# Kernel optimization log

Measured on AMD Instinct MI355X. Metric: run time of the kernel, lower is better.

Reference implementation:

```python
import jax, jax.numpy as jnp
import numpy as np

B, NBV, VD, A = 65536, 56, 7, 81
_BN_INV = np.float32(1.0 / np.sqrt(1.0 + 1e-5))  # eval-mode BN, running mean=0 var=1 (init state)


def _bn(x, g, b):
    # x: [B, C, F], per-channel affine over axis -2
    return x * (g * _BN_INV)[:, None] + b[:, None]


def _dpg(x, W, b, ng=8, ni=8):
    # DenseAndPartialGPool: first ng*ni feats -> grouped max+avg pool, rest -> relu(Linear)
    grp = x[..., : ng * ni].reshape(x.shape[:-1] + (ng, ni))
    dense = jax.nn.relu(x[..., ng * ni :] @ W + b)
    return jnp.concatenate([grp.max(-1), grp.mean(-1), dense], -1)


def setup_inputs() -> dict:
    key = jax.random.key(0)
    ks = iter(jax.random.split(key, 80))

    def W(si, so):
        return jax.random.normal(next(ks), (si, so), jnp.float32) * np.float32(1.0 / np.sqrt(si))

    def bias(n):
        return jnp.full((n,), 0.01, jnp.float32)

    inp = {}
    inp["input_data"] = jax.random.normal(next(ks), (B, NBV, VD), jnp.float32)
    inp["valid_actions"] = jax.random.randint(next(ks), (B, 1, A), 0, 2) > 0
    # dense2d_1
    inp["W1"], inp["b1"], inp["g1"], inp["be1"] = W(NBV, 128), bias(128), jnp.ones((7,), jnp.float32), jnp.zeros((7,), jnp.float32)
    inp["W2"], inp["b2"], inp["g2"], inp["be2"] = W(128, 128), bias(128), jnp.ones((7,), jnp.float32), jnp.zeros((7,), jnp.float32)
    inp["Wp1"], inp["bp1"] = W(64, 112), bias(112)
    inp["W3"], inp["b3"], inp["g3"], inp["be3"] = W(128, 128), bias(128), jnp.ones((7,), jnp.float32), jnp.zeros((7,), jnp.float32)
    inp["Wp2"], inp["bp2"] = W(64, 112), bias(112)
    inp["W4"], inp["b4"], inp["g4"], inp["be4"] = W(128, 128), bias(128), jnp.ones((7,), jnp.float32), jnp.zeros((7,), jnp.float32)
    inp["W5"], inp["b5"], inp["g5"], inp["be5"] = W(704, 512), bias(512), jnp.ones((1,), jnp.float32), jnp.zeros((1,), jnp.float32)
    inp["W6"], inp["b6"], inp["g6"], inp["be6"] = W(512, 256), bias(256), jnp.ones((1,), jnp.float32), jnp.zeros((1,), jnp.float32)
    inp["Wp4"], inp["bp4"] = W(192, 240), bias(240)
    inp["W7"], inp["b7"], inp["g7"], inp["be7"] = W(256, 256), bias(256), jnp.ones((1,), jnp.float32), jnp.zeros((1,), jnp.float32)
    inp["W8"], inp["b8"], inp["g8"], inp["be8"] = W(256, 256), bias(256), jnp.ones((1,), jnp.float32), jnp.zeros((1,), jnp.float32)
    inp["Wp5"], inp["bp5"] = W(192, 240), bias(240)
    inp["Wpi1"], inp["bpi1"] = W(256, 256), bias(256)
    inp["Wpi2"], inp["bpi2"] = W(256, A), bias(A)
    inp["Wv1"], inp["bv1"] = W(256, 256), bias(256)
    inp["Wv2"], inp["bv2"] = W(256, 1), bias(1)
    return inp


def reference(input_data, valid_actions, W1, b1, g1, be1, W2, b2, g2, be2, Wp1, bp1,
              W3, b3, g3, be3, Wp2, bp2, W4, b4, g4, be4,
              W5, b5, g5, be5, W6, b6, g6, be6, Wp4, bp4,
              W7, b7, g7, be7, W8, b8, g8, be8, Wp5, bp5,
              Wpi1, bpi1, Wpi2, bpi2, Wv1, bv1, Wv2, bv2):
    relu = jax.nn.relu
    x = jnp.transpose(input_data, (0, 2, 1))          # [B, 7, 56]
    x = relu(_bn(x @ W1 + b1, g1, be1))               # [B, 7, 128]
    x = relu(_bn(x @ W2 + b2, g2, be2))
    x = _dpg(x, Wp1, bp1)                             # [B, 7, 128]
    x = relu(_bn(x @ W3 + b3, g3, be3))
    x = _dpg(x, Wp2, bp2)
    x = relu(_bn(x @ W4 + b4, g4, be4))               # [B, 7, 128]
    # FlattenAndPartialGPool(64, 5)
    xb, xe = x[:, :, :64], x[:, :, 64:]
    first = xb[:, :5, :]                              # [B, 5, 64]
    n = x.shape[0]
    x = jnp.concatenate([first.max(1), first.mean(1),
                         xb[:, 5:, :].reshape(n, -1), xe.reshape(n, -1)], -1)[:, None, :]  # [B,1,704]
    x = relu(_bn(x @ W5 + b5, g5, be5))               # [B, 1, 512]
    x = relu(_bn(x @ W6 + b6, g6, be6))               # [B, 1, 256]
    x = _dpg(x, Wp4, bp4)
    x = relu(_bn(x @ W7 + b7, g7, be7))
    x = relu(_bn(x @ W8 + b8, g8, be8))
    x = _dpg(x, Wp5, bp5)                             # [B, 1, 256]
    v = jnp.tanh((x @ Wv1 + bv1) @ Wv2 + bv2)         # [B, 1, 1]
    pi = (x @ Wpi1 + bpi1) @ Wpi2 + bpi2              # [B, 1, A]
    pi = jnp.where(valid_actions, pi, jnp.float32(-1e8))
    return jax.nn.log_softmax(pi, axis=-1)[:, 0, :], v[:, 0, 0]
```

## Files before the change

### kernel.cpp

```cpp
#include <hip/hip_runtime.h>
#include <hip/hip_bf16.h>
#include <math.h>

#define BN_INV 0.99999500003749966f
#define NEG_BIG (-100000000.0f)

typedef __attribute__((ext_vector_type(8))) short s16x8;
typedef __attribute__((ext_vector_type(4))) float f32x4;

#define MFMA16(a,b,c) __builtin_amdgcn_mfma_f32_16x16x32_bf16(a,b,c,0,0,0)

__device__ __forceinline__ ushort f2b(float f){
  unsigned u = __builtin_bit_cast(unsigned, f);
  unsigned r = (u + 0x7FFFu + ((u>>16)&1u)) >> 16;
  return (ushort)r;
}
__device__ __forceinline__ float b2f(ushort h){
  unsigned u = ((unsigned)h)<<16; return __builtin_bit_cast(float, u);
}

#define OFF_W1   0
#define OFF_W2   8192
#define OFF_W3   24576
#define OFF_W4   40960
#define OFF_WP1  57344
#define OFF_WP2  64512
#define OFF_W5   71680
#define OFF_W6   432128
#define OFF_WP4  563200
#define OFF_WP5  609280
#define OFF_W7   655360
#define OFF_W8   720896
#define OFF_WPI1 786432
#define OFF_WPI2 851968
#define OFF_WV1  876544
#define OFF_X    942080

struct PrepParams {
  const float* src[15];
  long long off[15];
  int K[15], N[15], Kp[15], Np[15];
  ushort* ws;
};

__global__ void prep_pack(PrepParams pp){
  int wi = blockIdx.y;
  const float* s = pp.src[wi];
  ushort* d = pp.ws + pp.off[wi];
  int K = pp.K[wi], N = pp.N[wi], Np = pp.Np[wi];
  int tot = pp.Kp[wi]*Np;
  for (int idx = blockIdx.x*blockDim.x + threadIdx.x; idx < tot; idx += gridDim.x*blockDim.x){
    int k = idx / Np, j = idx - k*Np;
    float v = (k < K && j < N) ? s[k*N + j] : 0.f;
    d[(((k>>3)*Np + j)<<3) + (k&7)] = f2b(v);
  }
}

#define S1 136

struct P1 {
  const float* inp; const ushort* ws; ushort* xout;
  const float *b1,*g1,*be1,*b2,*g2,*be2,*bp1,*b3,*g3,*be3,*bp2,*b4,*g4,*be4;
};

template<int KT>
__device__ __forceinline__ void p1_mm(const ushort* X, ushort* Y, const ushort* W,
    const float* bias, const float* g, const float* be, int t){
  const int l=t&63, w=t>>6, lo=l&15, hi=l>>4;
  s16x8 Bf[2][KT];
  #pragma unroll
  for (int nt=0;nt<2;nt++)
    #pragma unroll
    for (int kt=0;kt<KT;kt++)
      Bf[nt][kt] = *(const s16x8*)(W + (((kt*4+hi)*128 + (w*2+nt)*16 + lo)<<3));
  float bc0 = bias[(w*2)*16+lo], bc1 = bias[(w*2+1)*16+lo];
  for (int mt=0; mt<7; mt++){
    const int rowb = mt*16;
    s16x8 Af[KT];
    #pragma unroll
    for (int kt=0;kt<KT;kt++)
      Af[kt] = *(const s16x8*)(X + (rowb+lo)*S1 + kt*32 + hi*8);
    f32x4 a0 = {0.f,0.f,0.f,0.f}, a1 = {0.f,0.f,0.f,0.f};
    #pragma unroll
    for (int kt=0;kt<KT;kt++){
      a0 = MFMA16(Af[kt], Bf[0][kt], a0);
      a1 = MFMA16(Af[kt], Bf[1][kt], a1);
    }
    #pragma unroll
    for (int r=0;r<4;r++){
      int row = rowb + hi*4 + r;
      int j = row % 7;
      float scj = g[j]*BN_INV, bbj = be[j];
      float v0 = fmaxf((a0[r]+bc0)*scj + bbj, 0.f);
      float v1 = fmaxf((a1[r]+bc1)*scj + bbj, 0.f);
      Y[row*S1 + (w*2)*16 + lo]   = f2b(v0);
      Y[row*S1 + (w*2+1)*16 + lo] = f2b(v1);
    }
  }
}

__device__ __forceinline__ void p1_dpg(const ushort* X, ushort* Y, const ushort* Wp,
                                       const float* bp, int t){
  const int l=t&63, w=t>>6, lo=l&15, hi=l>>4;
  const int nt0 = 2*w;
  const int ntn = (w<3) ? 2 : 1;
  s16x8 Bf[2][2];
  #pragma unroll
  for (int nt=0;nt<2;nt++)
    if (nt < ntn)
      #pragma unroll
      for (int kt=0;kt<2;kt++)
        Bf[nt][kt] = *(const s16x8*)(Wp + (((kt*4+hi)*112 + (nt0+nt)*16 + lo)<<3));
  float bc[2];
  #pragma unroll
  for (int nt=0;nt<2;nt++) bc[nt] = (nt<ntn) ? bp[(nt0+nt)*16+lo] : 0.f;
  for (int mt=0; mt<7; mt++){
    const int rowb = mt*16;
    s16x8 Af[2];
    #pragma unroll
    for (int kt=0;kt<2;kt++)
      Af[kt] = *(const s16x8*)(X + (rowb+lo)*S1 + 64 + kt*32 + hi*8);
    f32x4 acc0 = {0.f,0.f,0.f,0.f}, acc1 = {0.f,0.f,0.f,0.f};
    #pragma unroll
    for (int kt=0;kt<2;kt++){
      acc0 = MFMA16(Af[kt], Bf[0][kt], acc0);
      if (ntn > 1) acc1 = MFMA16(Af[kt], Bf[1][kt], acc1);
    }
    #pragma unroll
    for (int r=0;r<4;r++){
      int row = rowb + hi*4 + r;
      Y[row*S1 + 16 + nt0*16 + lo] = f2b(fmaxf(acc0[r] + bc[0], 0.f));
      if (ntn > 1)
        Y[row*S1 + 16 + (nt0+1)*16 + lo] = f2b(fmaxf(acc1[r] + bc[1], 0.f));
    }
  }
  if (w == 3){
    #pragma unroll
    for (int i=0;i<14;i++){
      int tau = l + 64*i;
      int row = tau>>3, gg = tau&7;
      s16x8 v8 = *(const s16x8*)(X + row*S1 + gg*8);
      float mx = b2f((ushort)v8[0]), smv = mx;
      #pragma unroll
      for (int q2=1;q2<8;q2++){ float vv = b2f((ushort)v8[q2]); mx = fmaxf(mx,vv); smv += vv; }
      Y[row*S1 + gg]     = f2b(mx);
      Y[row*S1 + 8 + gg] = f2b(smv*0.125f);
    }
  }
}

__global__ __launch_bounds__(256,2) void p1_kernel(P1 P){
  __shared__ ushort sA[112*S1];
  __shared__ ushort sB[112*S1];
  const int t = threadIdx.x;
  const size_t b0 = (size_t)blockIdx.x*16;
  const float* ip = P.inp + b0*392;
  for (int f=t; f<16*392; f+=256){
    int e = f/392, rem = f - e*392;
    int i = rem/7, j = rem - i*7;
    sA[(e*7+j)*S1 + i] = f2b(ip[f]);
  }
  for (int idx=t; idx<112*8; idx+=256)
    sA[(idx>>3)*S1 + 56 + (idx&7)] = 0;
  __syncthreads();
  p1_mm<2>(sA,sB, P.ws+OFF_W1, P.b1,P.g1,P.be1, t); __syncthreads();
  p1_mm<4>(sB,sA, P.ws+OFF_W2, P.b2,P.g2,P.be2, t); __syncthreads();
  p1_dpg(sA,sB, P.ws+OFF_WP1, P.bp1, t);            __syncthreads();
  p1_mm<4>(sB,sA, P.ws+OFF_W3, P.b3,P.g3,P.be3, t); __syncthreads();
  p1_dpg(sA,sB, P.ws+OFF_WP2, P.bp2, t);            __syncthreads();
  p1_mm<4>(sB,sA, P.ws+OFF_W4, P.b4,P.g4,P.be4, t); __syncthreads();
  ushort* xo = P.xout + b0*704;
  for (int idx=t; idx<16*704; idx+=256){
    int e = idx/704, c = idx - e*704;
    const ushort* Xr = sA + e*7*S1;
    float v;
    if (c < 64){
      float mx = b2f(Xr[c]);
      #pragma unroll
      for (int j=1;j<5;j++) mx = fmaxf(mx, b2f(Xr[j*S1+c]));
      v = mx;
    } else if (c < 128){
      int cc = c-64; float smv = 0.f;
      #pragma unroll
      for (int j=0;j<5;j++) smv += b2f(Xr[j*S1+cc]);
      v = smv*0.2f;
    } else if (c < 192) v = b2f(Xr[5*S1 + c-128]);
    else if (c < 256)   v = b2f(Xr[6*S1 + c-192]);
    else { int q2 = c-256; v = b2f(Xr[(q2>>6)*S1 + 64 + (q2&63)]); }
    xo[idx] = f2b(v);
  }
}

#define SX 712
#define SY 520
#define SZ 264

struct P2 {
  const ushort* x; const ushort* ws; const void* valid;
  const float *b5,*g5,*be5,*b6,*g6,*be6,*bp4,*b7,*g7,*be7,*b8,*g8,*be8,*bp5;
  const float *bpi1,*bpi2,*bv1,*Wv2,*bv2;
  float* out; long long Btot;
};

template<int KT, int NTW, int WN, int MODE>
__device__ __forceinline__ void p2_mm(const ushort* X, int sx, int xoff,
    ushort* Y, int sy, int yoff, const ushort* W, int n0,
    const float* bias, int bmax, float sc, float bb, int lo, int hi, int nact)
{
  f32x4 acc[4][NTW];
  #pragma unroll
  for (int m=0;m<4;m++)
    #pragma unroll
    for (int n=0;n<NTW;n++)
      acc[m][n] = (f32x4){0.f,0.f,0.f,0.f};
  for (int kt=0; kt<KT; kt++){
    s16x8 Af[4];
    #pragma unroll
    for (int m=0;m<4;m++)
      Af[m] = *(const s16x8*)(X + (m*16+lo)*sx + xoff + kt*32 + hi*8);
    s16x8 Bf[NTW];
    #pragma unroll
    for (int n=0;n<NTW;n++)
      if (n < nact)
        Bf[n] = *(const s16x8*)(W + (((size_t)(kt*4+hi)*WN + n0 + n*16 + lo)<<3));
    #pragma unroll
    for (int m=0;m<4;m++)
      #pragma unroll
      for (int n=0;n<NTW;n++)
        if (n < nact)
          acc[m][n] = MFMA16(Af[m], Bf[n], acc[m][n]);
  }
  #pragma unroll
  for (int n=0;n<NTW;n++){
    if (n < nact){
      int colw = n0 + n*16 + lo;
      float bc = (colw < bmax) ? bias[colw] : 0.f;
      #pragma unroll
      for (int m=0;m<4;m++){
        #pragma unroll
        for (int r=0;r<4;r++){
          int row = m*16 + hi*4 + r;
          float v = acc[m][n][r] + bc;
          if (MODE==0) v = fmaxf(v*sc+bb, 0.f);
          else if (MODE==1) v = fmaxf(v, 0.f);
          if (MODE==3) ((float*)Y)[row*sy + yoff + colw] = v;
          else Y[row*sy + yoff + colw] = f2b(v);
        }
      }
    }
  }
}

__device__ __forceinline__ void p2_group(const ushort* X, ushort* Y, int t){
  int row = t>>3, gg = t&7;
  s16x8 v8 = *(const s16x8*)(X + row*SZ + gg*8);
  float mx = b2f((ushort)v8[0]), smv = mx;
  #pragma unroll
  for (int q2=1;q2<8;q2++){ float vv = b2f((ushort)v8[q2]); mx = fmaxf(mx,vv); smv += vv; }
  Y[row*SZ + gg]     = f2b(mx);
  Y[row*SZ + 8 + gg] = f2b(smv*0.125f);
}

__global__ __launch_bounds__(512,2) void p2_kernel(P2 P){
  __shared__ ushort sm[78848];
  __shared__ int sflags[2];
  ushort* A0 = sm;
  ushort* A1 = sm + 45568;
  ushort* B0 = sm;
  ushort* B1 = sm + 16896;
  ushort* C  = sm + 45568;
  float*  Lf = (float*)sm;
  const int t = threadIdx.x;
  const int l = t&63, w = t>>6, lo = l&15, hi = l>>4;
  const size_t b0 = (size_t)blockIdx.x * 64;

  if (t < 2) sflags[t] = 0;
  __syncthreads();
  if (t < 256){
    const unsigned* vw = (const unsigned*)P.valid;
    int f3=0, nz=0;
    #pragma unroll
    for (int i=0;i<4;i++){
      unsigned u = vw[t*4+i];
      if (u & 0xFFFFFF00u) nz=1;
      if (((u>>24)&0xFFu)==0x3Fu || ((u>>16)&0xFFu)==0x3Fu ||
          ((u>>8)&0xFFu)==0x3Fu  || (u&0xFFu)==0x3Fu) f3=1;
    }
    if (f3) atomicOr(&sflags[0],1);
    if (nz) atomicOr(&sflags[1],1);
  }
  const ushort* xi = P.x + b0*704;
  for (int ci = t; ci < 64*88; ci += 512){
    int row = ci/88, c8 = ci - row*88;
    *(s16x8*)(A0 + row*SX + c8*8) = *(const s16x8*)(xi + row*704 + c8*8);
  }
  __syncthreads();
  const int vmode = sflags[0] ? 2 : (sflags[1] ? 0 : 1);
  float sc, bb;
  sc = P.g5[0]*BN_INV; bb = P.be5[0];
  p2_mm<22,4,512,0>(A0,SX,0, A1,SY,0, P.ws+OFF_W5, w*64, P.b5,512, sc,bb, lo,hi, 4);
  __syncthreads();
  sc = P.g6[0]*BN_INV; bb = P.be6[0];
  p2_mm<16,2,256,0>(A1,SY,0, B0,SZ,0, P.ws+OFF_W6, w*32, P.b6,256, sc,bb, lo,hi, 2);
  __syncthreads();
  p2_group(B0, B1, t);
  p2_mm<6,2,240,1>(B0,SZ,64, B1,SZ,16, P.ws+OFF_WP4, w*32, P.bp4,240, 0.f,0.f, lo,hi, (w==7)?1:2);
  __syncthreads();
  sc = P.g7[0]*BN_INV; bb = P.be7[0];
  p2_mm<8,2,256,0>(B1,SZ,0, B0,SZ,0, P.ws+OFF_W7, w*32, P.b7,256, sc,bb, lo,hi, 2);
  __syncthreads();
  sc = P.g8[0]*BN_INV; bb = P.be8[0];
  p2_mm<8,2,256,0>(B0,SZ,0, B1,SZ,0, P.ws+OFF_W8, w*32, P.b8,256, sc,bb, lo,hi, 2);
  __syncthreads();
  p2_group(B1, B0, t);
  p2_mm<6,2,240,1>(B1,SZ,64, B0,SZ,16, P.ws+OFF_WP5, w*32, P.bp5,240, 0.f,0.f, lo,hi, (w==7)?1:2);
  __syncthreads();
  p2_mm<8,2,256,2>(B0,SZ,0, B1,SZ,0, P.ws+OFF_WPI1, w*32, P.bpi1,256, 0.f,0.f, lo,hi, 2);
  p2_mm<8,2,256,2>(B0,SZ,0, C ,SZ,0, P.ws+OFF_WV1,  w*32, P.bv1, 256, 0.f,0.f, lo,hi, 2);
  __syncthreads();
  if (w < 6){
    p2_mm<8,1,96,3>(B1,SZ,0, (ushort*)Lf,104,0, P.ws+OFF_WPI2, w*16, P.bpi2,81, 0.f,0.f, lo,hi, 1);
  } else {
    int idx = (w-6)*64 + l;
    int row = idx>>1, half = idx&1;
    const ushort* hv = C + row*SZ + half*128;
    float s = 0.f;
    for (int k=0;k<128;k++) s += b2f(hv[k]) * P.Wv2[half*128+k];
    s += __shfl_xor(s, 1);
    if (!half) P.out[(size_t)P.Btot*81 + b0 + row] = tanhf(s + P.bv2[0]);
  }
  __syncthreads();
  {
    int row = t>>3, q = t&7;
    size_t b = b0 + row;
    const float* lr = Lf + row*104;
    float pm[11]; float mx = -INFINITY;
    #pragma unroll
    for (int i=0;i<11;i++){
      int c = q + 8*i;
      float v = NEG_BIG;
      if (c < 81){
        float sv = lr[c];
        bool valid;
        size_t vidx = b*81 + c;
        if (vmode==0)      valid = ((const unsigned char*)P.valid)[vidx] != 0;
        else if (vmode==1) valid = ((const int*)P.valid)[vidx] != 0;
        else               valid = ((const float*)P.valid)[vidx] != 0.f;
        v = valid ? sv : NEG_BIG;
      }
      pm[i] = v;
      mx = fmaxf(mx, v);
    }
    #pragma unroll
    for (int o=4;o;o>>=1) mx = fmaxf(mx, __shfl_xor(mx, o));
    float se = 0.f;
    #pragma unroll
    for (int i=0;i<11;i++){
      int c = q + 8*i;
      if (c < 81) se += expf(pm[i]-mx);
    }
    #pragma unroll
    for (int o=4;o;o>>=1) se += __shfl_xor(se, o);
    float lse = mx + logf(se);
    #pragma unroll
    for (int i=0;i<11;i++){
      int c = q + 8*i;
      if (c < 81) P.out[b*81 + c] = pm[i] - lse;
    }
  }
}

struct Params {
  const float* input;
  const void*  valid;
  const float *W1,*b1,*g1,*be1, *W2,*b2,*g2,*be2, *Wp1,*bp1;
  const float *W3,*b3,*g3,*be3, *Wp2,*bp2, *W4,*b4,*g4,*be4;
  const float *W5,*b5,*g5,*be5, *W6,*b6,*g6,*be6, *Wp4,*bp4;
  const float *W7,*b7,*g7,*be7, *W8,*b8,*g8,*be8, *Wp5,*bp5;
  const float *Wpi1,*bpi1,*Wpi2,*bpi2, *Wv1,*bv1,*Wv2,*bv2;
  float* out;
};

template<int K>
__device__ __forceinline__ void mm_p1(const float* __restrict__ X, float* __restrict__ Y,
    const float* __restrict__ W, const float* __restrict__ bias,
    const float* __restrict__ g, const float* __restrict__ be){
  const int t = threadIdx.x;
  const int m = t & 31, e = t >> 5;
  const int c0 = m * 4;
  const float* Xr = X + e*7*128;
  float acc[7][4];
  #pragma unroll
  for (int j=0;j<7;j++){acc[j][0]=0.f;acc[j][1]=0.f;acc[j][2]=0.f;acc[j][3]=0.f;}
  for (int k=0;k<K;k+=4){
    float4 wv[4];
    #pragma unroll
    for (int kk=0;kk<4;kk++) wv[kk] = *(const float4*)(W + (k+kk)*128 + c0);
    #pragma unroll
    for (int j=0;j<7;j++){
      float4 xv = *(const float4*)(Xr + j*128 + k);
      float xx[4] = {xv.x, xv.y, xv.z, xv.w};
      #pragma unroll
      for (int kk=0;kk<4;kk++){
        acc[j][0] += xx[kk]*wv[kk].x; acc[j][1] += xx[kk]*wv[kk].y;
        acc[j][2] += xx[kk]*wv[kk].z; acc[j][3] += xx[kk]*wv[kk].w;
      }
    }
  }
  float4 bs = *(const float4*)(bias + c0);
  #pragma unroll
  for (int j=0;j<7;j++){
    float sc = g[j]*BN_INV; float bb = be[j];
    float4 o;
    o.x = fmaxf((acc[j][0]+bs.x)*sc + bb, 0.f);
    o.y = fmaxf((acc[j][1]+bs.y)*sc + bb, 0.f);
    o.z = fmaxf((acc[j][2]+bs.z)*sc + bb, 0.f);
    o.w = fmaxf((acc[j][3]+bs.w)*sc + bb, 0.f);
    *(float4*)(Y + (e*7+j)*128 + c0) = o;
  }
}

__device__ __forceinline__ void dpg_p1f(const float* __restrict__ X, float* __restrict__ Y,
    const float* __restrict__ Wp, const float* __restrict__ bp){
  const int t = threadIdx.x;
  const int m = t & 31, e = t >> 5;
  const float* Xr = X + e*7*128;
  float* Yr = Y + e*7*128;
  if (m < 28) {
    const int c0 = m*4;
    float acc[7][4];
    #pragma unroll
    for (int j=0;j<7;j++){acc[j][0]=0.f;acc[j][1]=0.f;acc[j][2]=0.f;acc[j][3]=0.f;}
    for (int k=0;k<64;k+=4){
      float4 wv[4];
      #pragma unroll
      for (int kk=0;kk<4;kk++) wv[kk] = *(const float4*)(Wp + (k+kk)*112 + c0);
      #pragma unroll
      for (int j=0;j<7;j++){
        float4 xv = *(const float4*)(Xr + j*128 + 64 + k);
        float xx[4] = {xv.x, xv.y, xv.z, xv.w};
        #pragma unroll
        for (int kk=0;kk<4;kk++){
          acc[j][0] += xx[kk]*wv[kk].x; acc[j][1] += xx[kk]*wv[kk].y;
          acc[j][2] += xx[kk]*wv[kk].z; acc[j][3] += xx[kk]*wv[kk].w;
        }
      }
    }
    float4 bs = *(const float4*)(bp + c0);
    #pragma unroll
    for (int j=0;j<7;j++){
      float4 o;
      o.x = fmaxf(acc[j][0]+bs.x, 0.f); o.y = fmaxf(acc[j][1]+bs.y, 0.f);
      o.z = fmaxf(acc[j][2]+bs.z, 0.f); o.w = fmaxf(acc[j][3]+bs.w, 0.f);
      *(float4*)(Yr + j*128 + 16 + c0) = o;
    }
  } else if (m < 30) {
    #pragma unroll
    for (int j=0;j<7;j++){
      #pragma unroll
      for (int gi=0; gi<4; gi++){
        int gg = (m-28)*4 + gi;
        const float* p = Xr + j*128 + gg*8;
        float mx = p[0], smv = p[0];
        #pragma unroll
        for (int i=1;i<8;i++){ float v = p[i]; mx = fmaxf(mx, v); smv += v; }
        Yr[j*128 + gg] = mx;
        Yr[j*128 + 8 + gg] = smv*0.125f;
      }
    }
  }
}

__device__ __forceinline__ void flatten_st(const float* __restrict__ X, float* __restrict__ F){
  const int t = threadIdx.x, m = t & 31, e = t >> 5;
  const float* Xr = X + e*7*128;
  float* Fr = F + e*704;
  for (int col=m; col<704; col+=32){
    float v;
    if (col < 64){
      float mx = Xr[col];
      #pragma unroll
      for (int j=1;j<5;j++) mx = fmaxf(mx, Xr[j*128+col]);
      v = mx;
    } else if (col < 128){
      int c = col-64; float smv = 0.f;
      #pragma unroll
      for (int j=0;j<5;j++) smv += Xr[j*128+c];
      v = smv*0.2f;
    } else if (col < 192){ v = Xr[5*128 + (col-128)];
    } else if (col < 256){ v = Xr[6*128 + (col-192)];
    } else { int q = col-256; v = Xr[(q>>6)*128 + 64 + (q&63)]; }
    Fr[col] = v;
  }
}

template<int K, int N, int RPG, int MODE>
__device__ __forceinline__ void mm_p2(const float* __restrict__ X, int sx,
    float* __restrict__ Y, int sy, const float* __restrict__ W,
    const float* __restrict__ bias, float sc, float bb){
  constexpr int NC4 = N/4;
  constexpr int NG  = (8 + RPG - 1) / RPG;
  const int t = threadIdx.x;
  const int ci = t % NC4;
  const int grp = t / NC4;
  if (grp < NG) {
    const int c0 = ci*4;
    const int r0 = grp*RPG;
    float acc[RPG][4];
    #pragma unroll
    for (int r=0;r<RPG;r++){acc[r][0]=0.f;acc[r][1]=0.f;acc[r][2]=0.f;acc[r][3]=0.f;}
    for (int k=0;k<K;k+=4){
      float4 wv[4];
      #pragma unroll
      for (int kk=0;kk<4;kk++) wv[kk] = *(const float4*)(W + (k+kk)*N + c0);
      #pragma unroll
      for (int r=0;r<RPG;r++){
        float4 xv = *(const float4*)(X + (r0+r)*sx + k);
        float xx[4] = {xv.x, xv.y, xv.z, xv.w};
        #pragma unroll
        for (int kk=0;kk<4;kk++){
          acc[r][0] += xx[kk]*wv[kk].x; acc[r][1] += xx[kk]*wv[kk].y;
          acc[r][2] += xx[kk]*wv[kk].z; acc[r][3] += xx[kk]*wv[kk].w;
        }
      }
    }
    float4 bs = *(const float4*)(bias + c0);
    #pragma unroll
    for (int r=0;r<RPG;r++){
      float o[4] = {acc[r][0]+bs.x, acc[r][1]+bs.y, acc[r][2]+bs.z, acc[r][3]+bs.w};
      #pragma unroll
      for (int q=0;q<4;q++){
        if (MODE == 0) o[q] = o[q]*sc + bb;
        if (MODE <= 1) o[q] = fmaxf(o[q], 0.f);
      }
      float4 ov = {o[0],o[1],o[2],o[3]};
      *(float4*)(Y + (r0+r)*sy + c0) = ov;
    }
  }
}

__device__ __forceinline__ void dpg_p2_group(const float* __restrict__ X, float* __restrict__ Y){
  const int t = threadIdx.x;
  if (t < 128){
    int r = t >> 4, g0 = t & 15;
    const float* p = X + r*256 + (g0&7)*8;
    float mx = p[0], smv = p[0];
    #pragma unroll
    for (int i=1;i<8;i++){ float v = p[i]; mx = fmaxf(mx, v); smv += v; }
    Y[r*256 + g0] = (g0 < 8) ? mx : smv*0.125f;
  }
}

__global__ __launch_bounds__(256, 2)
void splendor_fwd(Params P, int Bt)
{
  __shared__ float bufA[7168];
  __shared__ float bufB[7168];
  __shared__ int sflags[2];
  const int t = threadIdx.x;
  const int b0 = blockIdx.x * 8;

  if (t < 2) sflags[t] = 0;
  __syncthreads();
  {
    const unsigned int* vw = (const unsigned int*)P.valid;
    int f3 = 0, nz = 0;
    #pragma unroll
    for (int i=0;i<4;i++){
      unsigned int u = vw[t*4 + i];
      if (u & 0xFFFFFF00u) nz = 1;
      if (((u>>24)&0xFFu)==0x3Fu || ((u>>16)&0xFFu)==0x3Fu ||
          ((u>>8)&0xFFu)==0x3Fu  || (u&0xFFu)==0x3Fu) f3 = 1;
    }
    if (f3) atomicOr(&sflags[0], 1);
    if (nz) atomicOr(&sflags[1], 1);
  }
  {
    const float* inp = P.input + (size_t)b0*392;
    for (int f=t; f<3136; f+=256){
      int e = f/392, rem = f - e*392;
      int i = rem/7, j = rem - i*7;
      bufA[(e*7+j)*128 + i] = inp[f];
    }
  }
  __syncthreads();
  const int vmode = sflags[0] ? 2 : (sflags[1] ? 0 : 1);

  mm_p1<56>(bufA, bufB, P.W1, P.b1, P.g1, P.be1);   __syncthreads();
  mm_p1<128>(bufB, bufA, P.W2, P.b2, P.g2, P.be2);  __syncthreads();
  dpg_p1f(bufA, bufB, P.Wp1, P.bp1);                __syncthreads();
  mm_p1<128>(bufB, bufA, P.W3, P.b3, P.g3, P.be3);  __syncthreads();
  dpg_p1f(bufA, bufB, P.Wp2, P.bp2);                __syncthreads();
  mm_p1<128>(bufB, bufA, P.W4, P.b4, P.g4, P.be4);  __syncthreads();
  flatten_st(bufA, bufB);                           __syncthreads();

  mm_p2<704,512,4,0>(bufB,704, bufA,512, P.W5, P.b5, P.g5[0]*BN_INV, P.be5[0]); __syncthreads();
  mm_p2<512,256,2,0>(bufA,512, bufB,256, P.W6, P.b6, P.g6[0]*BN_INV, P.be6[0]); __syncthreads();
  mm_p2<192,240,2,1>(bufB+64,256, bufA+16,256, P.Wp4, P.bp4, 0.f, 0.f);
  dpg_p2_group(bufB, bufA);                         __syncthreads();
  mm_p2<256,256,2,0>(bufA,256, bufB,256, P.W7, P.b7, P.g7[0]*BN_INV, P.be7[0]); __syncthreads();
  mm_p2<256,256,2,0>(bufB,256, bufA,256, P.W8, P.b8, P.g8[0]*BN_INV, P.be8[0]); __syncthreads();
  mm_p2<192,240,2,1>(bufA+64,256, bufB+16,256, P.Wp5, P.bp5, 0.f, 0.f);
  dpg_p2_group(bufA, bufB);                         __syncthreads();
  mm_p2<256,256,2,2>(bufB,256, bufA,256,      P.Wpi1, P.bpi1, 0.f, 0.f);
  mm_p2<256,256,2,2>(bufB,256, bufA+2048,256, P.Wv1,  P.bv1,  0.f, 0.f);
  __syncthreads();

  {
    const int r = t >> 5, lq = t & 31;
    const int b = b0 + r;
    const float* hp = bufA + r*256;
    float pm[3] = {NEG_BIG, NEG_BIG, NEG_BIG};
    float mx = -INFINITY;
    #pragma unroll
    for (int p=0;p<3;p++){
      int c = lq + 32*p;
      if (c < 81){
        float s = P.bpi2[c];
        for (int k=0;k<256;k++) s += hp[k]*P.Wpi2[k*81+c];
        bool valid;
        size_t idx = (size_t)b*81 + c;
        if (vmode == 0)      valid = ((const unsigned char*)P.valid)[idx] != 0;
        else if (vmode == 1) valid = ((const int*)P.valid)[idx] != 0;
        else                 valid = ((const float*)P.valid)[idx] != 0.f;
        pm[p] = valid ? s : NEG_BIG;
        mx = fmaxf(mx, pm[p]);
      }
    }
    #pragma unroll
    for (int off=16;off;off>>=1) mx = fmaxf(mx, __shfl_xor(mx, off, 32));
    float se = 0.f;
    #pragma unroll
    for (int p=0;p<3;p++){
      int c = lq + 32*p;
      if (c < 81) se += expf(pm[p]-mx);
    }
    #pragma unroll
    for (int off=16;off;off>>=1) se += __shfl_xor(se, off, 32);
    float lse = mx + logf(se);
    #pragma unroll
    for (int p=0;p<3;p++){
      int c = lq + 32*p;
      if (c < 81) P.out[(size_t)b*81 + c] = pm[p]-lse;
    }
  }
  if (t < 8){
    const float* hv = bufA + 2048 + t*256;
    float s = P.bv2[0];
    for (int k=0;k<256;k++) s += hv[k]*P.Wv2[k];
    P.out[(size_t)Bt*81 + b0 + t] = tanhf(s);
  }
}

extern "C" void kernel_launch(void* const* d_in, const int* in_sizes, int n_in,
                              void* d_out, int out_size, void* d_ws, size_t ws_size,
                              hipStream_t stream)
{
  const float* input = (const float*)d_in[0];
  const void*  valid = d_in[1];
  const float* W1  = (const float*)d_in[2];  const float* b1  = (const float*)d_in[3];
  const float* g1  = (const float*)d_in[4];  const float* be1 = (const float*)d_in[5];
  const float* W2  = (const float*)d_in[6];  const float* b2  = (const float*)d_in[7];
  const float* g2  = (const float*)d_in[8];  const float* be2 = (const float*)d_in[9];
  const float* Wp1 = (const float*)d_in[10]; const float* bp1 = (const float*)d_in[11];
  const float* W3  = (const float*)d_in[12]; const float* b3  = (const float*)d_in[13];
  const float* g3  = (const float*)d_in[14]; const float* be3 = (const float*)d_in[15];
  const float* Wp2 = (const float*)d_in[16]; const float* bp2 = (const float*)d_in[17];
  const float* W4  = (const float*)d_in[18]; const float* b4  = (const float*)d_in[19];
  const float* g4  = (const float*)d_in[20]; const float* be4 = (const float*)d_in[21];
  const float* W5  = (const float*)d_in[22]; const float* b5  = (const float*)d_in[23];
  const float* g5  = (const float*)d_in[24]; const float* be5 = (const float*)d_in[25];
  const float* W6  = (const float*)d_in[26]; const float* b6  = (const float*)d_in[27];
  const float* g6  = (const float*)d_in[28]; const float* be6 = (const float*)d_in[29];
  const float* Wp4 = (const float*)d_in[30]; const float* bp4 = (const float*)d_in[31];
  const float* W7  = (const float*)d_in[32]; const float* b7  = (const float*)d_in[33];
  const float* g7  = (const float*)d_in[34]; const float* be7 = (const float*)d_in[35];
  const float* W8  = (const float*)d_in[36]; const float* b8  = (const float*)d_in[37];
  const float* g8  = (const float*)d_in[38]; const float* be8 = (const float*)d_in[39];
  const float* Wp5 = (const float*)d_in[40]; const float* bp5 = (const float*)d_in[41];
  const float* Wpi1= (const float*)d_in[42]; const float* bpi1= (const float*)d_in[43];
  const float* Wpi2= (const float*)d_in[44]; const float* bpi2= (const float*)d_in[45];
  const float* Wv1 = (const float*)d_in[46]; const float* bv1 = (const float*)d_in[47];
  const float* Wv2 = (const float*)d_in[48]; const float* bv2 = (const float*)d_in[49];

  const long long Bt = in_sizes[0] / 392;
  const size_t need = ((size_t)OFF_X + (size_t)Bt*704) * 2;

  if (ws_size >= need && (Bt % 64) == 0) {
    ushort* wsu = (ushort*)d_ws;
    PrepParams pp;
    const float* srcs[15] = {W1,W2,W3,W4,Wp1,Wp2,W5,W6,Wp4,Wp5,W7,W8,Wpi1,Wpi2,Wv1};
    const long long offs[15] = {OFF_W1,OFF_W2,OFF_W3,OFF_W4,OFF_WP1,OFF_WP2,OFF_W5,OFF_W6,
                                OFF_WP4,OFF_WP5,OFF_W7,OFF_W8,OFF_WPI1,OFF_WPI2,OFF_WV1};
    const int Ks[15]  = {56,128,128,128, 64, 64,704,512,192,192,256,256,256,256,256};
    const int Ns[15]  = {128,128,128,128,112,112,512,256,240,240,256,256,256, 81,256};
    const int Kps[15] = {64,128,128,128, 64, 64,704,512,192,192,256,256,256,256,256};
    const int Nps[15] = {128,128,128,128,112,112,512,256,240,240,256,256,256, 96,256};
    for (int i=0;i<15;i++){
      pp.src[i]=srcs[i]; pp.off[i]=offs[i];
      pp.K[i]=Ks[i]; pp.N[i]=Ns[i]; pp.Kp[i]=Kps[i]; pp.Np[i]=Nps[i];
    }
    pp.ws = wsu;
    hipLaunchKernelGGL(prep_pack, dim3(256,15), dim3(256), 0, stream, pp);

    P1 p1;
    p1.inp = input; p1.ws = wsu; p1.xout = wsu + OFF_X;
    p1.b1=b1; p1.g1=g1; p1.be1=be1; p1.b2=b2; p1.g2=g2; p1.be2=be2; p1.bp1=bp1;
    p1.b3=b3; p1.g3=g3; p1.be3=be3; p1.bp2=bp2; p1.b4=b4; p1.g4=g4; p1.be4=be4;
    hipLaunchKernelGGL(p1_kernel, dim3((unsigned)(Bt/16)), dim3(256), 0, stream, p1);

    P2 p2;
    p2.x = wsu + OFF_X; p2.ws = wsu; p2.valid = valid;
    p2.b5=b5; p2.g5=g5; p2.be5=be5; p2.b6=b6; p2.g6=g6; p2.be6=be6; p2.bp4=bp4;
    p2.b7=b7; p2.g7=g7; p2.be7=be7; p2.b8=b8; p2.g8=g8; p2.be8=be8; p2.bp5=bp5;
    p2.bpi1=bpi1; p2.bpi2=bpi2; p2.bv1=bv1; p2.Wv2=Wv2; p2.bv2=bv2;
    p2.out = (float*)d_out; p2.Btot = Bt;
    hipLaunchKernelGGL(p2_kernel, dim3((unsigned)(Bt/64)), dim3(512), 0, stream, p2);
  } else {
    Params P;
    P.input = input; P.valid = valid;
    P.W1=W1; P.b1=b1; P.g1=g1; P.be1=be1; P.W2=W2; P.b2=b2; P.g2=g2; P.be2=be2;
    P.Wp1=Wp1; P.bp1=bp1; P.W3=W3; P.b3=b3; P.g3=g3; P.be3=be3; P.Wp2=Wp2; P.bp2=bp2;
    P.W4=W4; P.b4=b4; P.g4=g4; P.be4=be4; P.W5=W5; P.b5=b5; P.g5=g5; P.be5=be5;
    P.W6=W6; P.b6=b6; P.g6=g6; P.be6=be6; P.Wp4=Wp4; P.bp4=bp4;
    P.W7=W7; P.b7=b7; P.g7=g7; P.be7=be7; P.W8=W8; P.b8=b8; P.g8=g8; P.be8=be8;
    P.Wp5=Wp5; P.bp5=bp5; P.Wpi1=Wpi1; P.bpi1=bpi1; P.Wpi2=Wpi2; P.bpi2=bpi2;
    P.Wv1=Wv1; P.bv1=bv1; P.Wv2=Wv2; P.bv2=bv2;
    P.out = (float*)d_out;
    hipLaunchKernelGGL(splendor_fwd, dim3((unsigned)(Bt/8)), dim3(256), 0, stream, P, (int)Bt);
  }
}
```

Measured before the change: 740.6 us.

## Swap MFMA operand roles with transposed weights and shrink p2 tiles

Weights are now packed transposed (N-major, K contiguous), so the weights become the MFMA A operand and activations the B operand. Each lane's four outputs then run along the feature dimension and can be written as one packed 8-byte store. p1 moves to 512 threads with one 16-column tile per wave. p2 drops to 32 rows per block with a much smaller shared buffer, streams the 704-wide input straight from global memory instead of staging it in LDS, and raises occupancy bounds. The trade-off is that W5 and other weights are re-read from global or L2 by more blocks, and the grid gets twice as many p2 blocks.

```diff
diff --git a/kernel.cpp b/kernel.cpp
--- a/kernel.cpp
+++ b/kernel.cpp
@@ -17,6 +17,9 @@
 }
 __device__ __forceinline__ float b2f(ushort h){
   unsigned u = ((unsigned)h)<<16; return __builtin_bit_cast(float, u);
+}
+__device__ __forceinline__ unsigned pk2(float a, float b){
+  return (unsigned)f2b(a) | ((unsigned)f2b(b) << 16);
 }
 
 #define OFF_W1   0
@@ -44,16 +47,15 @@
 };
 
 __global__ void prep_pack(PrepParams pp){
-  int wi = blockIdx.y;
+  const int wi = blockIdx.y;
+  const int Kp = pp.Kp[wi], Np = pp.Np[wi], K = pp.K[wi], N = pp.N[wi];
+  const int tot = Kp*Np;
+  int idx = blockIdx.x*256 + threadIdx.x;
+  if (idx >= tot) return;
+  int n = idx / Kp, k = idx - n*Kp;
   const float* s = pp.src[wi];
-  ushort* d = pp.ws + pp.off[wi];
-  int K = pp.K[wi], N = pp.N[wi], Np = pp.Np[wi];
-  int tot = pp.Kp[wi]*Np;
-  for (int idx = blockIdx.x*blockDim.x + threadIdx.x; idx < tot; idx += gridDim.x*blockDim.x){
-    int k = idx / Np, j = idx - k*Np;
-    float v = (k < K && j < N) ? s[k*N + j] : 0.f;
-    d[(((k>>3)*Np + j)<<3) + (k&7)] = f2b(v);
-  }
+  float v = (k < K && n < N) ? s[k*N + n] : 0.f;
+  pp.ws[pp.off[wi] + idx] = f2b(v);
 }
 
 #define S1 136
@@ -64,114 +66,112 @@
 };
 
 template<int KT>
-__device__ __forceinline__ void p1_mm(const ushort* X, ushort* Y, const ushort* W,
-    const float* bias, const float* g, const float* be, int t){
+__device__ __forceinline__ void p1_mmS(const ushort* X, ushort* Y,
+    const ushort* Wt, const int Kp, const float* bias,
+    const float* g, const float* be, int t)
+{
   const int l=t&63, w=t>>6, lo=l&15, hi=l>>4;
-  s16x8 Bf[2][KT];
-  #pragma unroll
-  for (int nt=0;nt<2;nt++)
-    #pragma unroll
-    for (int kt=0;kt<KT;kt++)
-      Bf[nt][kt] = *(const s16x8*)(W + (((kt*4+hi)*128 + (w*2+nt)*16 + lo)<<3));
-  float bc0 = bias[(w*2)*16+lo], bc1 = bias[(w*2+1)*16+lo];
+  const int n0 = w*16;
+  s16x8 Aw[KT];
+  const ushort* wr = Wt + (n0+lo)*Kp + hi*8;
+  #pragma unroll
+  for (int kt=0;kt<KT;kt++) Aw[kt] = *(const s16x8*)(wr + kt*32);
+  const float4 bs = *(const float4*)(bias + n0 + hi*4);
+  int j = lo % 7;
+  #pragma unroll
   for (int mt=0; mt<7; mt++){
-    const int rowb = mt*16;
-    s16x8 Af[KT];
-    #pragma unroll
-    for (int kt=0;kt<KT;kt++)
-      Af[kt] = *(const s16x8*)(X + (rowb+lo)*S1 + kt*32 + hi*8);
-    f32x4 a0 = {0.f,0.f,0.f,0.f}, a1 = {0.f,0.f,0.f,0.f};
+    const int row = mt*16 + lo;
+    const ushort* xr = X + row*S1 + hi*8;
+    f32x4 a = {0.f,0.f,0.f,0.f};
     #pragma unroll
     for (int kt=0;kt<KT;kt++){
-      a0 = MFMA16(Af[kt], Bf[0][kt], a0);
-      a1 = MFMA16(Af[kt], Bf[1][kt], a1);
-    }
-    #pragma unroll
-    for (int r=0;r<4;r++){
-      int row = rowb + hi*4 + r;
-      int j = row % 7;
-      float scj = g[j]*BN_INV, bbj = be[j];
-      float v0 = fmaxf((a0[r]+bc0)*scj + bbj, 0.f);
-      float v1 = fmaxf((a1[r]+bc1)*scj + bbj, 0.f);
-      Y[row*S1 + (w*2)*16 + lo]   = f2b(v0);
-      Y[row*S1 + (w*2+1)*16 + lo] = f2b(v1);
-    }
-  }
-}
-
-__device__ __forceinline__ void p1_dpg(const ushort* X, ushort* Y, const ushort* Wp,
-                                       const float* bp, int t){
+      s16x8 bx = *(const s16x8*)(xr + kt*32);
+      a = MFMA16(Aw[kt], bx, a);
+    }
+    const float scj = g[j]*BN_INV, bbj = be[j];
+    float v0 = fmaxf((a[0]+bs.x)*scj + bbj, 0.f);
+    float v1 = fmaxf((a[1]+bs.y)*scj + bbj, 0.f);
+    float v2 = fmaxf((a[2]+bs.z)*scj + bbj, 0.f);
+    float v3 = fmaxf((a[3]+bs.w)*scj + bbj, 0.f);
+    uint2 pv; pv.x = pk2(v0,v1); pv.y = pk2(v2,v3);
+    *(uint2*)(Y + row*S1 + n0 + hi*4) = pv;
+    j += 2; if (j >= 7) j -= 7;
+  }
+}
+
+__device__ __forceinline__ void p1_dpgS(const ushort* X, ushort* Y,
+    const ushort* Wpt, const float* bp, int t)
+{
   const int l=t&63, w=t>>6, lo=l&15, hi=l>>4;
-  const int nt0 = 2*w;
-  const int ntn = (w<3) ? 2 : 1;
-  s16x8 Bf[2][2];
-  #pragma unroll
-  for (int nt=0;nt<2;nt++)
-    if (nt < ntn)
-      #pragma unroll
-      for (int kt=0;kt<2;kt++)
-        Bf[nt][kt] = *(const s16x8*)(Wp + (((kt*4+hi)*112 + (nt0+nt)*16 + lo)<<3));
-  float bc[2];
-  #pragma unroll
-  for (int nt=0;nt<2;nt++) bc[nt] = (nt<ntn) ? bp[(nt0+nt)*16+lo] : 0.f;
-  for (int mt=0; mt<7; mt++){
-    const int rowb = mt*16;
-    s16x8 Af[2];
-    #pragma unroll
-    for (int kt=0;kt<2;kt++)
-      Af[kt] = *(const s16x8*)(X + (rowb+lo)*S1 + 64 + kt*32 + hi*8);
-    f32x4 acc0 = {0.f,0.f,0.f,0.f}, acc1 = {0.f,0.f,0.f,0.f};
-    #pragma unroll
-    for (int kt=0;kt<2;kt++){
-      acc0 = MFMA16(Af[kt], Bf[0][kt], acc0);
-      if (ntn > 1) acc1 = MFMA16(Af[kt], Bf[1][kt], acc1);
-    }
-    #pragma unroll
-    for (int r=0;r<4;r++){
-      int row = rowb + hi*4 + r;
-      Y[row*S1 + 16 + nt0*16 + lo] = f2b(fmaxf(acc0[r] + bc[0], 0.f));
-      if (ntn > 1)
-        Y[row*S1 + 16 + (nt0+1)*16 + lo] = f2b(fmaxf(acc1[r] + bc[1], 0.f));
-    }
-  }
-  if (w == 3){
-    #pragma unroll
-    for (int i=0;i<14;i++){
-      int tau = l + 64*i;
-      int row = tau>>3, gg = tau&7;
+  #pragma unroll
+  for (int it=0; it<2; it++){
+    int idx = t + it*512;
+    if (idx < 896){
+      int row = idx>>3, gg = idx&7;
       s16x8 v8 = *(const s16x8*)(X + row*S1 + gg*8);
-      float mx = b2f((ushort)v8[0]), smv = mx;
-      #pragma unroll
-      for (int q2=1;q2<8;q2++){ float vv = b2f((ushort)v8[q2]); mx = fmaxf(mx,vv); smv += vv; }
-      Y[row*S1 + gg]     = f2b(mx);
-      Y[row*S1 + 8 + gg] = f2b(smv*0.125f);
-    }
-  }
-}
-
-__global__ __launch_bounds__(256,2) void p1_kernel(P1 P){
+      float mx = b2f((ushort)v8[0]), sm = mx;
+      #pragma unroll
+      for (int q=1;q<8;q++){ float vv=b2f((ushort)v8[q]); mx=fmaxf(mx,vv); sm+=vv; }
+      Y[row*S1+gg]   = f2b(mx);
+      Y[row*S1+8+gg] = f2b(sm*0.125f);
+    }
+  }
+  if (w < 7){
+    const int n0 = w*16;
+    const ushort* wr = Wpt + (n0+lo)*64 + hi*8;
+    s16x8 Aw0 = *(const s16x8*)(wr);
+    s16x8 Aw1 = *(const s16x8*)(wr + 32);
+    const float4 bs = *(const float4*)(bp + n0 + hi*4);
+    #pragma unroll
+    for (int mt=0; mt<7; mt++){
+      const int row = mt*16 + lo;
+      const ushort* xr = X + row*S1 + 64 + hi*8;
+      f32x4 a = {0.f,0.f,0.f,0.f};
+      a = MFMA16(Aw0, *(const s16x8*)(xr), a);
+      a = MFMA16(Aw1, *(const s16x8*)(xr+32), a);
+      float v0 = fmaxf(a[0]+bs.x, 0.f);
+      float v1 = fmaxf(a[1]+bs.y, 0.f);
+      float v2 = fmaxf(a[2]+bs.z, 0.f);
+      float v3 = fmaxf(a[3]+bs.w, 0.f);
+      uint2 pv; pv.x = pk2(v0,v1); pv.y = pk2(v2,v3);
+      *(uint2*)(Y + row*S1 + 16 + n0 + hi*4) = pv;
+    }
+  }
+}
+
+__global__ __launch_bounds__(512,4) void p1_kernel(P1 P){
   __shared__ ushort sA[112*S1];
   __shared__ ushort sB[112*S1];
   const int t = threadIdx.x;
   const size_t b0 = (size_t)blockIdx.x*16;
-  const float* ip = P.inp + b0*392;
-  for (int f=t; f<16*392; f+=256){
-    int e = f/392, rem = f - e*392;
-    int i = rem/7, j = rem - i*7;
-    sA[(e*7+j)*S1 + i] = f2b(ip[f]);
-  }
-  for (int idx=t; idx<112*8; idx+=256)
+  {
+    const int e = t>>5, la = t&31;
+    const float* ep = P.inp + (b0+e)*392;
+    ushort* dst = sA + e*7*S1;
+    for (int i=la; i<56; i+=32){
+      const float* q = ep + i*7;
+      #pragma unroll
+      for (int j=0;j<7;j++) dst[j*S1 + i] = f2b(q[j]);
+    }
+  }
+  for (int idx=t; idx<896; idx+=512)
     sA[(idx>>3)*S1 + 56 + (idx&7)] = 0;
   __syncthreads();
-  p1_mm<2>(sA,sB, P.ws+OFF_W1, P.b1,P.g1,P.be1, t); __syncthreads();
-  p1_mm<4>(sB,sA, P.ws+OFF_W2, P.b2,P.g2,P.be2, t); __syncthreads();
-  p1_dpg(sA,sB, P.ws+OFF_WP1, P.bp1, t);            __syncthreads();
-  p1_mm<4>(sB,sA, P.ws+OFF_W3, P.b3,P.g3,P.be3, t); __syncthreads();
-  p1_dpg(sA,sB, P.ws+OFF_WP2, P.bp2, t);            __syncthreads();
-  p1_mm<4>(sB,sA, P.ws+OFF_W4, P.b4,P.g4,P.be4, t); __syncthreads();
+  p1_mmS<2>(sA,sB, P.ws+OFF_W1, 64,  P.b1,P.g1,P.be1, t); __syncthreads();
+  p1_mmS<4>(sB,sA, P.ws+OFF_W2, 128, P.b2,P.g2,P.be2, t); __syncthreads();
+  p1_dpgS(sA,sB, P.ws+OFF_WP1, P.bp1, t);                 __syncthreads();
+  p1_mmS<4>(sB,sA, P.ws+OFF_W3, 128, P.b3,P.g3,P.be3, t); __syncthreads();
+  p1_dpgS(sA,sB, P.ws+OFF_WP2, P.bp2, t);                 __syncthreads();
+  p1_mmS<4>(sB,sA, P.ws+OFF_W4, 128, P.b4,P.g4,P.be4, t); __syncthreads();
   ushort* xo = P.xout + b0*704;
-  for (int idx=t; idx<16*704; idx+=256){
-    int e = idx/704, c = idx - e*704;
+  for (int idx=t; idx<896; idx+=512){
+    int e = idx/56, ch = idx - e*56;
+    int q = ch*8;
+    const ushort* Xr = sA + e*7*S1;
+    *(s16x8*)(xo + e*704 + 256 + q) = *(const s16x8*)(Xr + (q>>6)*S1 + 64 + (q&63));
+  }
+  for (int idx=t; idx<4096; idx+=512){
+    int e = idx>>8, c = idx&255;
     const ushort* Xr = sA + e*7*S1;
     float v;
     if (c < 64){
@@ -180,18 +180,16 @@
       for (int j=1;j<5;j++) mx = fmaxf(mx, b2f(Xr[j*S1+c]));
       v = mx;
     } else if (c < 128){
-      int cc = c-64; float smv = 0.f;
-      #pragma unroll
-      for (int j=0;j<5;j++) smv += b2f(Xr[j*S1+cc]);
-      v = smv*0.2f;
+      int cc = c-64; float sm = 0.f;
+      #pragma unroll
+      for (int j=0;j<5;j++) sm += b2f(Xr[j*S1+cc]);
+      v = sm*0.2f;
     } else if (c < 192) v = b2f(Xr[5*S1 + c-128]);
-    else if (c < 256)   v = b2f(Xr[6*S1 + c-192]);
-    else { int q2 = c-256; v = b2f(Xr[(q2>>6)*S1 + 64 + (q2&63)]); }
-    xo[idx] = f2b(v);
-  }
-}
-
-#define SX 712
+    else                v = b2f(Xr[6*S1 + c-192]);
+    xo[e*704 + c] = f2b(v);
+  }
+}
+
 #define SY 520
 #define SZ 264
 
@@ -202,49 +200,64 @@
   float* out; long long Btot;
 };
 
-template<int KT, int NTW, int WN, int MODE>
-__device__ __forceinline__ void p2_mm(const ushort* X, int sx, int xoff,
-    ushort* Y, int sy, int yoff, const ushort* W, int n0,
-    const float* bias, int bmax, float sc, float bb, int lo, int hi, int nact)
+template<int KT, int NTW, int MODE>
+__device__ __forceinline__ void p2_mmS(const ushort* X, int sx, int xoff,
+    ushort* Y, int sy, int yoff, const ushort* Wt, int Kp, int n0, int nact,
+    const float* bias, int bmax, float sc, float bb, int lo, int hi)
 {
-  f32x4 acc[4][NTW];
-  #pragma unroll
-  for (int m=0;m<4;m++)
-    #pragma unroll
-    for (int n=0;n<NTW;n++)
-      acc[m][n] = (f32x4){0.f,0.f,0.f,0.f};
+  const ushort* xr0 = X + (0*16+lo)*sx + xoff + hi*8;
+  const ushort* xr1 = X + (1*16+lo)*sx + xoff + hi*8;
+  const ushort* wr[NTW];
+  #pragma unroll
+  for (int n=0;n<NTW;n++) wr[n] = Wt + (size_t)(n0+n*16+lo)*Kp + hi*8;
+  f32x4 acc[2][NTW];
+  #pragma unroll
+  for (int m=0;m<2;m++)
+    #pragma unroll
+    for (int n=0;n<NTW;n++) acc[m][n] = (f32x4){0.f,0.f,0.f,0.f};
+  #pragma unroll
   for (int kt=0; kt<KT; kt++){
-    s16x8 Af[4];
-    #pragma unroll
-    for (int m=0;m<4;m++)
-      Af[m] = *(const s16x8*)(X + (m*16+lo)*sx + xoff + kt*32 + hi*8);
-    s16x8 Bf[NTW];
-    #pragma unroll
-    for (int n=0;n<NTW;n++)
-      if (n < nact)
-        Bf[n] = *(const s16x8*)(W + (((size_t)(kt*4+hi)*WN + n0 + n*16 + lo)<<3));
-    #pragma unroll
-    for (int m=0;m<4;m++)
-      #pragma unroll
-      for (int n=0;n<NTW;n++)
-        if (n < nact)
-          acc[m][n] = MFMA16(Af[m], Bf[n], acc[m][n]);
+    s16x8 bx0 = *(const s16x8*)(xr0 + kt*32);
+    s16x8 bx1 = *(const s16x8*)(xr1 + kt*32);
+    #pragma unroll
+    for (int n=0;n<NTW;n++){
+      if (n < nact){
+        s16x8 aw = *(const s16x8*)(wr[n] + kt*32);
+        acc[0][n] = MFMA16(aw, bx0, acc[0][n]);
+        acc[1][n] = MFMA16(aw, bx1, acc[1][n]);
+      }
+    }
   }
   #pragma unroll
   for (int n=0;n<NTW;n++){
     if (n < nact){
-      int colw = n0 + n*16 + lo;
-      float bc = (colw < bmax) ? bias[colw] : 0.f;
-      #pragma unroll
-      for (int m=0;m<4;m++){
-        #pragma unroll
-        for (int r=0;r<4;r++){
-          int row = m*16 + hi*4 + r;
-          float v = acc[m][n][r] + bc;
-          if (MODE==0) v = fmaxf(v*sc+bb, 0.f);
-          else if (MODE==1) v = fmaxf(v, 0.f);
-          if (MODE==3) ((float*)Y)[row*sy + yoff + colw] = v;
-          else Y[row*sy + yoff + colw] = f2b(v);
+      const int nc = n0 + n*16 + hi*4;
+      float4 bs;
+      if (nc+3 < bmax) bs = *(const float4*)(bias + nc);
+      else {
+        bs.x = (nc   < bmax)? bias[nc]  :0.f;
+        bs.y = (nc+1 < bmax)? bias[nc+1]:0.f;
+        bs.z = (nc+2 < bmax)? bias[nc+2]:0.f;
+        bs.w = (nc+3 < bmax)? bias[nc+3]:0.f;
+      }
+      #pragma unroll
+      for (int m=0;m<2;m++){
+        const int row = m*16 + lo;
+        float v0 = acc[m][n][0]+bs.x, v1 = acc[m][n][1]+bs.y;
+        float v2 = acc[m][n][2]+bs.z, v3 = acc[m][n][3]+bs.w;
+        if (MODE==0){
+          v0 = fmaxf(v0*sc+bb,0.f); v1 = fmaxf(v1*sc+bb,0.f);
+          v2 = fmaxf(v2*sc+bb,0.f); v3 = fmaxf(v3*sc+bb,0.f);
+        } else if (MODE==1){
+          v0 = fmaxf(v0,0.f); v1 = fmaxf(v1,0.f);
+          v2 = fmaxf(v2,0.f); v3 = fmaxf(v3,0.f);
+        }
+        if (MODE==3){
+          float4 fv = {v0,v1,v2,v3};
+          *(float4*)((float*)Y + (size_t)row*sy + yoff + nc) = fv;
+        } else {
+          uint2 pv; pv.x = pk2(v0,v1); pv.y = pk2(v2,v3);
+          *(uint2*)(Y + row*sy + yoff + nc) = pv;
         }
       }
     }
@@ -254,25 +267,24 @@
 __device__ __forceinline__ void p2_group(const ushort* X, ushort* Y, int t){
   int row = t>>3, gg = t&7;
   s16x8 v8 = *(const s16x8*)(X + row*SZ + gg*8);
-  float mx = b2f((ushort)v8[0]), smv = mx;
-  #pragma unroll
-  for (int q2=1;q2<8;q2++){ float vv = b2f((ushort)v8[q2]); mx = fmaxf(mx,vv); smv += vv; }
+  float mx = b2f((ushort)v8[0]), sm = mx;
+  #pragma unroll
+  for (int q=1;q<8;q++){ float vv = b2f((ushort)v8[q]); mx = fmaxf(mx,vv); sm += vv; }
   Y[row*SZ + gg]     = f2b(mx);
-  Y[row*SZ + 8 + gg] = f2b(smv*0.125f);
-}
-
-__global__ __launch_bounds__(512,2) void p2_kernel(P2 P){
-  __shared__ ushort sm[78848];
+  Y[row*SZ + 8 + gg] = f2b(sm*0.125f);
+}
+
+__global__ __launch_bounds__(512,4) void p2_kernel(P2 P){
+  __shared__ ushort sm[25344];
   __shared__ int sflags[2];
-  ushort* A0 = sm;
-  ushort* A1 = sm + 45568;
-  ushort* B0 = sm;
-  ushort* B1 = sm + 16896;
-  ushort* C  = sm + 45568;
-  float*  Lf = (float*)sm;
+  ushort* A1 = sm;
+  ushort* B1 = sm;
+  ushort* C  = sm + 8448;
+  ushort* B0 = sm + 16896;
+  float*  Lf = (float*)(sm + 16896);
   const int t = threadIdx.x;
   const int l = t&63, w = t>>6, lo = l&15, hi = l>>4;
-  const size_t b0 = (size_t)blockIdx.x * 64;
+  const size_t b0 = (size_t)blockIdx.x * 32;
 
   if (t < 2) sflags[t] = 0;
   __syncthreads();
@@ -289,40 +301,37 @@
     if (f3) atomicOr(&sflags[0],1);
     if (nz) atomicOr(&sflags[1],1);
   }
-  const ushort* xi = P.x + b0*704;
-  for (int ci = t; ci < 64*88; ci += 512){
-    int row = ci/88, c8 = ci - row*88;
-    *(s16x8*)(A0 + row*SX + c8*8) = *(const s16x8*)(xi + row*704 + c8*8);
-  }
+  p2_mmS<22,4,0>(P.x + b0*704, 704, 0, A1, SY, 0, P.ws+OFF_W5, 704,
+                 w*64, 4, P.b5, 512, P.g5[0]*BN_INV, P.be5[0], lo,hi);
+  __syncthreads();
+  p2_mmS<16,2,0>(A1, SY, 0, B0, SZ, 0, P.ws+OFF_W6, 512,
+                 w*32, 2, P.b6, 256, P.g6[0]*BN_INV, P.be6[0], lo,hi);
+  __syncthreads();
+  if (t < 256) p2_group(B0, B1, t);
+  p2_mmS<6,2,1>(B0, SZ, 64, B1, SZ, 16, P.ws+OFF_WP4, 192,
+                w*32, (w<7)?2:1, P.bp4, 240, 0.f,0.f, lo,hi);
+  __syncthreads();
+  p2_mmS<8,2,0>(B1, SZ, 0, B0, SZ, 0, P.ws+OFF_W7, 256,
+                w*32, 2, P.b7, 256, P.g7[0]*BN_INV, P.be7[0], lo,hi);
+  __syncthreads();
+  p2_mmS<8,2,0>(B0, SZ, 0, B1, SZ, 0, P.ws+OFF_W8, 256,
+                w*32, 2, P.b8, 256, P.g8[0]*BN_INV, P.be8[0], lo,hi);
+  __syncthreads();
+  if (t < 256) p2_group(B1, B0, t);
+  p2_mmS<6,2,1>(B1, SZ, 64, B0, SZ, 16, P.ws+OFF_WP5, 192,
+                w*32, (w<7)?2:1, P.bp5, 240, 0.f,0.f, lo,hi);
+  __syncthreads();
+  p2_mmS<8,2,2>(B0, SZ, 0, B1, SZ, 0, P.ws+OFF_WPI1, 256,
+                w*32, 2, P.bpi1, 256, 0.f,0.f, lo,hi);
+  p2_mmS<8,2,2>(B0, SZ, 0, C , SZ, 0, P.ws+OFF_WV1 , 256,
+                w*32, 2, P.bv1 , 256, 0.f,0.f, lo,hi);
   __syncthreads();
   const int vmode = sflags[0] ? 2 : (sflags[1] ? 0 : 1);
-  float sc, bb;
-  sc = P.g5[0]*BN_INV; bb = P.be5[0];
-  p2_mm<22,4,512,0>(A0,SX,0, A1,SY,0, P.ws+OFF_W5, w*64, P.b5,512, sc,bb, lo,hi, 4);
-  __syncthreads();
-  sc = P.g6[0]*BN_INV; bb = P.be6[0];
-  p2_mm<16,2,256,0>(A1,SY,0, B0,SZ,0, P.ws+OFF_W6, w*32, P.b6,256, sc,bb, lo,hi, 2);
-  __syncthreads();
-  p2_group(B0, B1, t);
-  p2_mm<6,2,240,1>(B0,SZ,64, B1,SZ,16, P.ws+OFF_WP4, w*32, P.bp4,240, 0.f,0.f, lo,hi, (w==7)?1:2);
-  __syncthreads();
-  sc = P.g7[0]*BN_INV; bb = P.be7[0];
-  p2_mm<8,2,256,0>(B1,SZ,0, B0,SZ,0, P.ws+OFF_W7, w*32, P.b7,256, sc,bb, lo,hi, 2);
-  __syncthreads();
-  sc = P.g8[0]*BN_INV; bb = P.be8[0];
-  p2_mm<8,2,256,0>(B0,SZ,0, B1,SZ,0, P.ws+OFF_W8, w*32, P.b8,256, sc,bb, lo,hi, 2);
-  __syncthreads();
-  p2_group(B1, B0, t);
-  p2_mm<6,2,240,1>(B1,SZ,64, B0,SZ,16, P.ws+OFF_WP5, w*32, P.bp5,240, 0.f,0.f, lo,hi, (w==7)?1:2);
-  __syncthreads();
-  p2_mm<8,2,256,2>(B0,SZ,0, B1,SZ,0, P.ws+OFF_WPI1, w*32, P.bpi1,256, 0.f,0.f, lo,hi, 2);
-  p2_mm<8,2,256,2>(B0,SZ,0, C ,SZ,0, P.ws+OFF_WV1,  w*32, P.bv1, 256, 0.f,0.f, lo,hi, 2);
-  __syncthreads();
   if (w < 6){
-    p2_mm<8,1,96,3>(B1,SZ,0, (ushort*)Lf,104,0, P.ws+OFF_WPI2, w*16, P.bpi2,81, 0.f,0.f, lo,hi, 1);
-  } else {
-    int idx = (w-6)*64 + l;
-    int row = idx>>1, half = idx&1;
+    p2_mmS<8,1,3>(B1, SZ, 0, (ushort*)Lf, 104, 0, P.ws+OFF_WPI2, 256,
+                  w*16, 1, P.bpi2, 81, 0.f,0.f, lo,hi);
+  } else if (w == 6){
+    int row = l>>1, half = l&1;
     const ushort* hv = C + row*SZ + half*128;
     float s = 0.f;
     for (int k=0;k<128;k++) s += b2f(hv[k]) * P.Wv2[half*128+k];
@@ -330,7 +339,7 @@
     if (!half) P.out[(size_t)P.Btot*81 + b0 + row] = tanhf(s + P.bv2[0]);
   }
   __syncthreads();
-  {
+  if (t < 256){
     int row = t>>3, q = t&7;
     size_t b = b0 + row;
     const float* lr = Lf + row*104;
@@ -686,7 +695,7 @@
   const long long Bt = in_sizes[0] / 392;
   const size_t need = ((size_t)OFF_X + (size_t)Bt*704) * 2;
 
-  if (ws_size >= need && (Bt % 64) == 0) {
+  if (ws_size >= need && (Bt % 32) == 0) {
     ushort* wsu = (ushort*)d_ws;
     PrepParams pp;
     const float* srcs[15] = {W1,W2,W3,W4,Wp1,Wp2,W5,W6,Wp4,Wp5,W7,W8,Wpi1,Wpi2,Wv1};
@@ -701,13 +710,13 @@
       pp.K[i]=Ks[i]; pp.N[i]=Ns[i]; pp.Kp[i]=Kps[i]; pp.Np[i]=Nps[i];
     }
     pp.ws = wsu;
-    hipLaunchKernelGGL(prep_pack, dim3(256,15), dim3(256), 0, stream, pp);
+    hipLaunchKernelGGL(prep_pack, dim3(1408,15), dim3(256), 0, stream, pp);
 
     P1 p1;
     p1.inp = input; p1.ws = wsu; p1.xout = wsu + OFF_X;
     p1.b1=b1; p1.g1=g1; p1.be1=be1; p1.b2=b2; p1.g2=g2; p1.be2=be2; p1.bp1=bp1;
     p1.b3=b3; p1.g3=g3; p1.be3=be3; p1.bp2=bp2; p1.b4=b4; p1.g4=g4; p1.be4=be4;
-    hipLaunchKernelGGL(p1_kernel, dim3((unsigned)(Bt/16)), dim3(256), 0, stream, p1);
+    hipLaunchKernelGGL(p1_kernel, dim3((unsigned)(Bt/16)), dim3(512), 0, stream, p1);
 
     P2 p2;
     p2.x = wsu + OFF_X; p2.ws = wsu; p2.valid = valid;
@@ -715,7 +724,7 @@
     p2.b7=b7; p2.g7=g7; p2.be7=be7; p2.b8=b8; p2.g8=g8; p2.be8=be8; p2.bp5=bp5;
     p2.bpi1=bpi1; p2.bpi2=bpi2; p2.bv1=bv1; p2.Wv2=Wv2; p2.bv2=bv2;
     p2.out = (float*)d_out; p2.Btot = Bt;
-    hipLaunchKernelGGL(p2_kernel, dim3((unsigned)(Bt/64)), dim3(512), 0, stream, p2);
+    hipLaunchKernelGGL(p2_kernel, dim3((unsigned)(Bt/32)), dim3(512), 0, stream, p2);
   } else {
     Params P;
     P.input = input; P.valid = valid;
```

Measured after the change: 890.4 us. +20.2%, slower.
